# Performance work log

Hardware: AMD Instinct MI355X
Metric: run time of the kernel (lower is better)

The kernel has to match this reference:

```python
import jax, jax.numpy as jnp
import numpy as np

N_NODES = 10000
N_EDGES = 160000
HIDDEN = 128
NGAUSS = 100
NF = 64
N_CONV = 2


def setup_inputs() -> dict:
    key = jax.random.key(0)
    ks = jax.random.split(key, 10)
    h = jax.random.normal(ks[0], (N_NODES, HIDDEN), dtype=jnp.float32)
    edge_index = jax.random.randint(ks[1], (2, N_EDGES), 0, N_NODES, dtype=jnp.int64)
    edge_weight = jax.random.uniform(ks[2], (N_EDGES,), dtype=jnp.float32)
    edge_attr = jax.random.normal(ks[3], (N_EDGES, NGAUSS), dtype=jnp.float32)
    data = jnp.zeros((1,), dtype=jnp.float32)
    s = 0.05
    lin0_w = jax.random.normal(ks[4], (HIDDEN, NF), dtype=jnp.float32) * s
    lin0_b = jnp.zeros((NF,), dtype=jnp.float32)
    nn_w1 = jax.random.normal(ks[5], (NGAUSS, HIDDEN), dtype=jnp.float32) * s
    nn_b1 = jnp.zeros((HIDDEN,), dtype=jnp.float32)
    nn_w2 = jax.random.normal(ks[6], (HIDDEN, NF * NF), dtype=jnp.float32) * s
    nn_b2 = jnp.zeros((NF * NF,), dtype=jnp.float32)
    root_w = jax.random.normal(ks[7], (NF, NF), dtype=jnp.float32) * s
    conv_b = jnp.zeros((NF,), dtype=jnp.float32)
    return {"h": h, "edge_index": edge_index, "edge_weight": edge_weight,
            "edge_attr": edge_attr, "data": data,
            "lin0_w": lin0_w, "lin0_b": lin0_b,
            "nn_w1": nn_w1, "nn_b1": nn_b1, "nn_w2": nn_w2, "nn_b2": nn_b2,
            "root_w": root_w, "conv_b": conv_b}


def reference(h, edge_index, edge_weight, edge_attr, data,
              lin0_w, lin0_b, nn_w1, nn_b1, nn_w2, nn_b2, root_w, conv_b):
    # lin0 + relu -> node features x: [N, nf]
    x = jax.nn.relu(h @ lin0_w + lin0_b)

    # edge network: per-edge weight matrix W_e: [E, nf, nf]
    hidden = jax.nn.relu(edge_attr @ nn_w1 + nn_b1)
    W_e = (hidden @ nn_w2 + nn_b2).reshape(N_EDGES, NF, NF)

    src = edge_index[0]  # message source (x_j)
    dst = edge_index[1]  # aggregation target (i)

    # in-degree for mean aggregation (0-degree nodes -> 0 output)
    deg = jax.ops.segment_sum(jnp.ones((N_EDGES,), x.dtype), dst, num_segments=N_NODES)
    inv_deg = (1.0 / jnp.maximum(deg, 1.0))[:, None]  # [N, 1]

    # n_conv applications of the SAME NNConv (shared weights)
    for _ in range(N_CONV):
        msg = jnp.einsum('ei,eio->eo', x[src], W_e)  # gather + per-edge matvec
        agg = jax.ops.segment_sum(msg, dst, num_segments=N_NODES) * inv_deg
        x = agg + x @ root_w + conv_b
    return x
```

## Files before the change

### kernel.cpp

```cpp
#include <hip/hip_runtime.h>

#define N_NODES 10000
#define N_EDGES 160000
#define HID 128
#define NG 100
#define NF 64
#define NIO 4096
#define NJ 8192
#define M_PAD 10240

typedef short bf16x8 __attribute__((ext_vector_type(8)));
typedef float f32x4 __attribute__((ext_vector_type(4)));

__device__ __forceinline__ unsigned short f2b(float f) {
    unsigned int u = __float_as_uint(f);
    u += 0x7fffu + ((u >> 16) & 1u);
    return (unsigned short)(u >> 16);
}
__device__ __forceinline__ float b2f(unsigned short s) { return __uint_as_float((unsigned int)s << 16); }

__device__ __forceinline__ long fidx64(int row, int k) {
    return (long)(row >> 4) * 1024 + (k >> 5) * 512 + ((((k >> 3) & 3) * 16 + (row & 15))) * 8 + (k & 7);
}
__device__ __forceinline__ long fidx128(int row, int k) {
    return (long)(row >> 4) * 2048 + (k >> 5) * 512 + ((((k >> 3) & 3) * 16 + (row & 15))) * 8 + (k & 7);
}

__global__ void hist_kernel(const int* __restrict__ src, const int* __restrict__ dst,
                            float* __restrict__ deg, int* __restrict__ cnt) {
    int e = blockIdx.x * 256 + threadIdx.x;
    if (e < N_EDGES) {
        atomicAdd(&deg[dst[e]], 1.0f);
        atomicAdd(&cnt[src[e]], 1);
    }
}

#define SCAN_C 40
__global__ void scan_kernel(const int* __restrict__ cnt, const float* __restrict__ deg,
                            int* __restrict__ rowptr, float* __restrict__ invd) {
    __shared__ int wsum[4];
    int t = threadIdx.x, wv = t >> 6, l = t & 63;
    int base_i = t * SCAN_C;
    int loc[SCAN_C];
    int sum = 0;
#pragma unroll
    for (int j = 0; j < SCAN_C; ++j) {
        int g = base_i + j;
        int v = (g < N_NODES) ? cnt[g] : 0;
        loc[j] = sum;
        sum += v;
    }
    int incl = sum;
    for (int off = 1; off < 64; off <<= 1) {
        int v = __shfl_up(incl, off);
        if (l >= off) incl += v;
    }
    if (l == 63) wsum[wv] = incl;
    __syncthreads();
    int wbase = 0;
#pragma unroll
    for (int w = 0; w < 4; ++w) wbase += (w < wv) ? wsum[w] : 0;
    int tbase = wbase + incl - sum;
#pragma unroll
    for (int j = 0; j < SCAN_C; ++j) {
        int g = base_i + j;
        if (g <= N_NODES) rowptr[g] = tbase + loc[j];
        if (g < N_NODES) invd[g] = 1.0f / fmaxf(deg[g], 1.0f);
    }
}

__global__ void scatter_kernel(const int* __restrict__ src, const int* __restrict__ dst,
                               const int* __restrict__ rowptr, int* __restrict__ fill,
                               int* __restrict__ edgeOf, int* __restrict__ dstp) {
    int e = blockIdx.x * 256 + threadIdx.x;
    if (e < N_EDGES) {
        int s = src[e];
        int r = rowptr[s] + atomicAdd(&fill[s], 1);
        edgeOf[r] = e;
        dstp[r] = dst[e];
    }
}

__global__ void lin0_kernel(const float* __restrict__ h, const float* __restrict__ w,
                            const float* __restrict__ b, const float* __restrict__ b2,
                            float* __restrict__ x, unsigned short* __restrict__ xh,
                            float* __restrict__ xb2) {
    int wv = threadIdx.x >> 6, l = threadIdx.x & 63;
    int n = blockIdx.x * 4 + wv;
    float h0 = h[n * HID + l];
    float h1 = h[n * HID + 64 + l];
    float acc = b[l];
#pragma unroll
    for (int i = 0; i < 64; ++i) {
        acc += __shfl(h0, i) * w[i * NF + l];
        acc += __shfl(h1, i) * w[(64 + i) * NF + l];
    }
    float v = fmaxf(acc, 0.0f);
    x[n * NF + l] = v;
    xh[fidx64(n, l)] = f2b(v);
    float xb = 0.0f;
#pragma unroll
    for (int i = 0; i < 64; ++i) xb += __shfl(v, i) * b2[i * 64 + l];
    xb2[n * NF + l] = xb;
}

__global__ void eaperm_kernel(const float* __restrict__ ea, const int* __restrict__ edgeOf,
                              unsigned short* __restrict__ eah) {
    int t = threadIdx.x;
    int r15 = t & 15, ksl = t >> 4;
    int ks = ksl >> 2, lk = ksl & 3;
    long rank = (long)blockIdx.x * 16 + r15;
    long e = edgeOf[rank];
    int c0 = ks * 32 + lk * 8;
    unsigned int uh[4];
#pragma unroll
    for (int p = 0; p < 4; ++p) {
        float v0 = (c0 + 2 * p < NG) ? ea[e * NG + c0 + 2 * p] : 0.0f;
        float v1 = (c0 + 2 * p + 1 < NG) ? ea[e * NG + c0 + 2 * p + 1] : 0.0f;
        uh[p] = ((unsigned int)f2b(v1) << 16) | f2b(v0);
    }
    long idx = (long)blockIdx.x * 2048 + ks * 512 + (lk * 16 + r15) * 8;
    *(uint4*)(eah + idx) = make_uint4(uh[0], uh[1], uh[2], uh[3]);
}

__global__ void wpt_kernel(const float* __restrict__ w1, const float* __restrict__ w2,
                           unsigned short* __restrict__ w1h, unsigned short* __restrict__ w2h) {
    int id = blockIdx.x * 256 + threadIdx.x;
    if (id < HID * HID) {
        int k = id & 127, c = id >> 7;
        float v = (k < NG) ? w1[k * HID + c] : 0.0f;
        w1h[fidx128(c, k)] = f2b(v);
    } else {
        int id2 = id - HID * HID;
        int i = id2 & 63, j = id2 >> 6;
        int o = j >> 7, k = j & 127;
        w2h[fidx64(j, i)] = f2b(w2[k * NIO + i * 64 + o]);
    }
}

__launch_bounds__(256)
__global__ void hgemm_kernel(const unsigned short* __restrict__ eah,
                             const unsigned short* __restrict__ w1h,
                             const float* __restrict__ b1, unsigned short* __restrict__ hidp) {
    __shared__ float stg[4][1056];
    const int tid = threadIdx.x, wv = tid >> 6, l = tid & 63;
    const long grow = (long)blockIdx.x * 128;
    const int wr = (wv >> 1) * 64, wc = (wv & 1) * 64;
    const long apan0 = (grow >> 4) + (wr >> 4);
    const long bpan0 = (wc >> 4);

    f32x4 acc[4][4] = {};
#pragma unroll
    for (int ks = 0; ks < 4; ++ks) {
        bf16x8 a[4], b[4];
#pragma unroll
        for (int m = 0; m < 4; ++m)
            a[m] = *(const bf16x8*)(eah + (apan0 + m) * 2048 + ks * 512 + (long)l * 8);
#pragma unroll
        for (int n = 0; n < 4; ++n)
            b[n] = *(const bf16x8*)(w1h + (bpan0 + n) * 2048 + ks * 512 + (long)l * 8);
#pragma unroll
        for (int m = 0; m < 4; ++m)
#pragma unroll
            for (int n = 0; n < 4; ++n)
                acc[m][n] = __builtin_amdgcn_mfma_f32_16x16x32_bf16(a[m], b[n], acc[m][n], 0, 0, 0);
    }

    float* s = stg[wv];
    int r8 = l >> 3, cg = l & 7;
#pragma unroll
    for (int m = 0; m < 4; ++m) {
#pragma unroll
        for (int n = 0; n < 4; ++n)
#pragma unroll
            for (int q = 0; q < 4; ++q)
                s[((l >> 4) * 4 + q) * 66 + n * 16 + (l & 15)] = acc[m][n][q];
#pragma unroll
        for (int it = 0; it < 2; ++it) {
            int row = it * 8 + r8;
            const float* sr = s + row * 66 + cg * 8;
            int colbase = wc + cg * 8;
            unsigned int u[4];
#pragma unroll
            for (int p = 0; p < 4; ++p) {
                float f0 = fmaxf(sr[2 * p] + b1[colbase + 2 * p], 0.0f);
                float f1 = fmaxf(sr[2 * p + 1] + b1[colbase + 2 * p + 1], 0.0f);
                u[p] = ((unsigned int)f2b(f1) << 16) | f2b(f0);
            }
            long R = grow + wr + m * 16 + row;
            *(uint4*)(hidp + R * HID + colbase) = make_uint4(u[0], u[1], u[2], u[3]);
        }
    }
}

__launch_bounds__(256)
__global__ void ygemm_kernel(const unsigned short* __restrict__ xh,
                             const unsigned short* __restrict__ wh,
                             unsigned short* __restrict__ y, int n0) {
    __shared__ float stg[4][1056];
    const int tid = threadIdx.x, wv = tid >> 6, l = tid & 63;
    const int grow = blockIdx.x * 128;
    const int col0 = blockIdx.y * 128;
    const int wr = (wv >> 1) * 64, wc = (wv & 1) * 64;
    const long apan0 = ((n0 + grow + wr) >> 4);
    const long bpan0 = ((col0 + wc) >> 4);

    f32x4 acc[4][4] = {};
#pragma unroll
    for (int ks = 0; ks < 2; ++ks) {
        bf16x8 a[4], b[4];
#pragma unroll
        for (int m = 0; m < 4; ++m)
            a[m] = *(const bf16x8*)(xh + (apan0 + m) * 1024 + ks * 512 + (long)l * 8);
#pragma unroll
        for (int n = 0; n < 4; ++n)
            b[n] = *(const bf16x8*)(wh + (bpan0 + n) * 1024 + ks * 512 + (long)l * 8);
#pragma unroll
        for (int m = 0; m < 4; ++m)
#pragma unroll
            for (int n = 0; n < 4; ++n)
                acc[m][n] = __builtin_amdgcn_mfma_f32_16x16x32_bf16(a[m], b[n], acc[m][n], 0, 0, 0);
    }

    float* s = stg[wv];
    int r8 = l >> 3, cg = l & 7;
#pragma unroll
    for (int m = 0; m < 4; ++m) {
#pragma unroll
        for (int n = 0; n < 4; ++n)
#pragma unroll
            for (int q = 0; q < 4; ++q)
                s[((l >> 4) * 4 + q) * 66 + n * 16 + (l & 15)] = acc[m][n][q];
#pragma unroll
        for (int it = 0; it < 2; ++it) {
            int row = it * 8 + r8;
            const float* sr = s + row * 66 + cg * 8;
            unsigned int u[4];
#pragma unroll
            for (int p = 0; p < 4; ++p)
                u[p] = ((unsigned int)f2b(sr[2 * p + 1]) << 16) | f2b(sr[2 * p]);
            long R = grow + wr + m * 16 + row;
            *(uint4*)(y + R * NJ + col0 + wc + cg * 8) = make_uint4(u[0], u[1], u[2], u[3]);
        }
    }
}

__global__ void matvec_mfma_kernel(const unsigned short* __restrict__ y,
                                   const unsigned short* __restrict__ hidp,
                                   const int* __restrict__ rowptr, const int* __restrict__ dstp,
                                   const float* __restrict__ xb2, float* __restrict__ agg,
                                   int n0) {
    int wv = threadIdx.x >> 6, l = threadIdx.x & 63;
    int s = n0 + blockIdx.x;
    int r0 = rowptr[s], r1 = rowptr[s + 1];
    if (r0 == r1) return;
    int co = wv * 16;
    int lc = l & 15, lk = l >> 4;

    const unsigned short* Ys = y + (long)(s - n0) * NJ + (co + lc) * HID;
    bf16x8 b[4];
#pragma unroll
    for (int ks = 0; ks < 4; ++ks) b[ks] = *(const bf16x8*)(Ys + ks * 32 + lk * 8);
    float xb2v = xb2[(long)s * NF + co + lc];

    for (int mt = r0; mt < r1; mt += 16) {
        const unsigned short* Hs = hidp + (long)(mt + lc) * HID + lk * 8;
        f32x4 acc = {};
#pragma unroll
        for (int ks = 0; ks < 4; ++ks) {
            bf16x8 a = *(const bf16x8*)(Hs + ks * 32);
            acc = __builtin_amdgcn_mfma_f32_16x16x32_bf16(a, b[ks], acc, 0, 0, 0);
        }
#pragma unroll
        for (int q = 0; q < 4; ++q) {
            int rank = mt + lk * 4 + q;
            if (rank < r1) {
                int dd = dstp[rank];
                atomicAdd(&agg[(long)dd * NF + co + lc], acc[q] + xb2v);
            }
        }
    }
}

__global__ void combine_kernel(const float* __restrict__ x, const float* __restrict__ agg,
                               const float* __restrict__ invd, const float* __restrict__ rw,
                               const float* __restrict__ cb, const float* __restrict__ b2,
                               float* __restrict__ xo, unsigned short* __restrict__ xh,
                               float* __restrict__ xb2) {
    int wv = threadIdx.x >> 6, l = threadIdx.x & 63;
    int n = blockIdx.x * 4 + wv;
    float xv = x[n * NF + l];
    float acc = cb[l];
#pragma unroll
    for (int i = 0; i < 64; ++i) acc += __shfl(xv, i) * rw[i * NF + l];
    float v = agg[n * NF + l] * invd[n] + acc;
    xo[n * NF + l] = v;
    if (xh) {
        xh[fidx64(n, l)] = f2b(v);
        float xb = 0.0f;
#pragma unroll
        for (int i = 0; i < 64; ++i) xb += __shfl(v, i) * b2[i * 64 + l];
        xb2[n * NF + l] = xb;
    }
}

extern "C" void kernel_launch(void* const* d_in, const int* in_sizes, int n_in,
                              void* d_out, int out_size, void* d_ws, size_t ws_size,
                              hipStream_t stream) {
    const float* h = (const float*)d_in[0];
    const int* ei = (const int*)d_in[1];
    const float* ea = (const float*)d_in[3];
    const float* lin0_w = (const float*)d_in[5];
    const float* lin0_b = (const float*)d_in[6];
    const float* nn_w1 = (const float*)d_in[7];
    const float* nn_b1 = (const float*)d_in[8];
    const float* nn_w2 = (const float*)d_in[9];
    const float* nn_b2 = (const float*)d_in[10];
    const float* root_w = (const float*)d_in[11];
    const float* conv_b = (const float*)d_in[12];
    const int* srcIdx = ei;
    const int* dstIdx = ei + N_EDGES;

    const size_t eaBytes = (size_t)N_EDGES * HID * 2;
    const size_t fixed =
        (size_t)(N_EDGES + 16) * HID * 2 +
        (size_t)NJ * NF * 2 +
        (size_t)HID * HID * 2 +
        (size_t)M_PAD * NF * 2 +
        (size_t)N_NODES * NF * 4 * 4 +
        3 * 40192 +
        (size_t)N_NODES * 4 +
        (size_t)(N_NODES + 1) * 4 +
        (size_t)N_EDGES * 4 * 2 +
        32768;
    int nc = 0, CSn = 0;
    size_t region_bytes = 0;
    for (int c = 2; c <= 16; c *= 2) {
        int csn = (((N_NODES + c - 1) / c) + 127) & ~127;
        size_t rb = (size_t)csn * NJ * 2;
        if (rb < eaBytes) rb = eaBytes;
        if (fixed + rb <= ws_size) { nc = c; CSn = csn; region_bytes = rb; break; }
    }
    if (nc == 0) {
        hipMemsetAsync(d_out, 0, (size_t)out_size * 4, stream);
        return;
    }

    char* ws = (char*)d_ws;
    size_t off = 0;
    auto alloc = [&](size_t bytes) {
        char* p = ws + off;
        off += (bytes + 255) & ~(size_t)255;
        return p;
    };
    unsigned short* region = (unsigned short*)alloc(region_bytes);
    unsigned short* y = region;
    unsigned short* eah = region;
    unsigned short* hidp = (unsigned short*)alloc((size_t)(N_EDGES + 16) * HID * 2);
    unsigned short* w2h = (unsigned short*)alloc((size_t)NJ * NF * 2);
    unsigned short* w1h = (unsigned short*)alloc((size_t)HID * HID * 2);
    unsigned short* xh = (unsigned short*)alloc((size_t)M_PAD * NF * 2);
    float* xA = (float*)alloc((size_t)N_NODES * NF * 4);
    float* xB = (float*)alloc((size_t)N_NODES * NF * 4);
    float* agg = (float*)alloc((size_t)N_NODES * NF * 4);
    float* xb2 = (float*)alloc((size_t)N_NODES * NF * 4);
    char* degblk = alloc(3 * 40192);
    float* deg = (float*)degblk;
    int* cnt = (int*)(degblk + 40192);
    int* fill = (int*)(degblk + 2 * 40192);
    float* invd = (float*)alloc((size_t)N_NODES * 4);
    int* rowptr = (int*)alloc((size_t)(N_NODES + 1) * 4);
    int* edgeOf = (int*)alloc((size_t)N_EDGES * 4);
    int* dstp = (int*)alloc((size_t)N_EDGES * 4);

    hipMemsetAsync(degblk, 0, 3 * 40192, stream);
    hist_kernel<<<(N_EDGES + 255) / 256, 256, 0, stream>>>(srcIdx, dstIdx, deg, cnt);
    scan_kernel<<<1, 256, 0, stream>>>(cnt, deg, rowptr, invd);
    scatter_kernel<<<(N_EDGES + 255) / 256, 256, 0, stream>>>(srcIdx, dstIdx, rowptr, fill, edgeOf, dstp);
    lin0_kernel<<<N_NODES / 4, 256, 0, stream>>>(h, lin0_w, lin0_b, nn_b2, xA, xh, xb2);
    eaperm_kernel<<<N_EDGES / 16, 256, 0, stream>>>(ea, edgeOf, eah);
    wpt_kernel<<<(HID * HID + NJ * NF) / 256, 256, 0, stream>>>(nn_w1, nn_w2, w1h, w2h);
    hgemm_kernel<<<N_EDGES / 128, 256, 0, stream>>>(eah, w1h, nn_b1, hidp);

    for (int conv = 0; conv < 2; ++conv) {
        const float* xin = conv ? xB : xA;
        float* xout = conv ? (float*)d_out : xB;
        unsigned short* mh = conv ? nullptr : xh;

        hipMemsetAsync(agg, 0, (size_t)N_NODES * NF * 4, stream);
        for (int c = 0; c < nc; ++c) {
            int n0 = c * CSn;
            int n1 = n0 + CSn; if (n1 > N_NODES) n1 = N_NODES;
            if (n0 >= N_NODES) break;
            int gx = (n1 - n0 + 127) / 128;
            ygemm_kernel<<<dim3(gx, NJ / 128), 256, 0, stream>>>(xh, w2h, y, n0);
            matvec_mfma_kernel<<<n1 - n0, 256, 0, stream>>>(y, hidp, rowptr, dstp, xb2, agg, n0);
        }
        combine_kernel<<<N_NODES / 4, 256, 0, stream>>>(xin, agg, invd, root_w, conv_b, nn_b2,
                                                        xout, mh, xb2);
    }
}
```

Before: 371.5 us.

## Fuse per-node weight GEMM and edge matvec into one panel kernel

Replaces the chunked ygemm plus matvec launch pairs with a single kernel of 157 blocks. Each block computes the y (per-node projected weight) rows for a 64-node panel across all 8192 columns, then runs the MFMA matvec and atomic scatter for those same nodes. The aim is to remove per-chunk launch overhead and to reuse freshly written y data from cache. The cost is far less parallelism: fewer blocks than compute units, the column tiles and nodes are processed serially inside each block, and a full-size y buffer is required in the workspace.

```diff
diff --git a/kernel.cpp b/kernel.cpp
--- a/kernel.cpp
+++ b/kernel.cpp
@@ -8,6 +8,7 @@
 #define NIO 4096
 #define NJ 8192
 #define M_PAD 10240
+#define NPANEL 157
 
 typedef short bf16x8 __attribute__((ext_vector_type(8)));
 typedef float f32x4 __attribute__((ext_vector_type(4)));
@@ -194,89 +195,86 @@
 }
 
 __launch_bounds__(256)
-__global__ void ygemm_kernel(const unsigned short* __restrict__ xh,
-                             const unsigned short* __restrict__ wh,
-                             unsigned short* __restrict__ y, int n0) {
+__global__ void conv_fused_kernel(const unsigned short* __restrict__ xh,
+                                  const unsigned short* __restrict__ w2h,
+                                  const unsigned short* __restrict__ hidp,
+                                  const int* __restrict__ rowptr, const int* __restrict__ dstp,
+                                  const float* __restrict__ xb2, float* __restrict__ agg,
+                                  unsigned short* __restrict__ y) {
     __shared__ float stg[4][1056];
     const int tid = threadIdx.x, wv = tid >> 6, l = tid & 63;
-    const int grow = blockIdx.x * 128;
-    const int col0 = blockIdx.y * 128;
-    const int wr = (wv >> 1) * 64, wc = (wv & 1) * 64;
-    const long apan0 = ((n0 + grow + wr) >> 4);
-    const long bpan0 = ((col0 + wc) >> 4);
-
-    f32x4 acc[4][4] = {};
-#pragma unroll
-    for (int ks = 0; ks < 2; ++ks) {
-        bf16x8 a[4], b[4];
-#pragma unroll
-        for (int m = 0; m < 4; ++m)
-            a[m] = *(const bf16x8*)(xh + (apan0 + m) * 1024 + ks * 512 + (long)l * 8);
-#pragma unroll
-        for (int n = 0; n < 4; ++n)
-            b[n] = *(const bf16x8*)(wh + (bpan0 + n) * 1024 + ks * 512 + (long)l * 8);
-#pragma unroll
-        for (int m = 0; m < 4; ++m)
+    const int p0 = blockIdx.x * 64;
+    const long apan0 = (p0 >> 4);
+    const int r8 = l >> 3, cg = l & 7;
+
+    for (int ct = 0; ct < 32; ++ct) {
+        const int colW = ct * 256 + wv * 64;
+        const long bpan0 = (colW >> 4);
+        f32x4 acc[4][4] = {};
+#pragma unroll
+        for (int ks = 0; ks < 2; ++ks) {
+            bf16x8 a[4], b[4];
+#pragma unroll
+            for (int m = 0; m < 4; ++m)
+                a[m] = *(const bf16x8*)(xh + (apan0 + m) * 1024 + ks * 512 + (long)l * 8);
 #pragma unroll
             for (int n = 0; n < 4; ++n)
-                acc[m][n] = __builtin_amdgcn_mfma_f32_16x16x32_bf16(a[m], b[n], acc[m][n], 0, 0, 0);
-    }
-
-    float* s = stg[wv];
-    int r8 = l >> 3, cg = l & 7;
-#pragma unroll
-    for (int m = 0; m < 4; ++m) {
-#pragma unroll
-        for (int n = 0; n < 4; ++n)
-#pragma unroll
-            for (int q = 0; q < 4; ++q)
-                s[((l >> 4) * 4 + q) * 66 + n * 16 + (l & 15)] = acc[m][n][q];
-#pragma unroll
-        for (int it = 0; it < 2; ++it) {
-            int row = it * 8 + r8;
-            const float* sr = s + row * 66 + cg * 8;
-            unsigned int u[4];
-#pragma unroll
-            for (int p = 0; p < 4; ++p)
-                u[p] = ((unsigned int)f2b(sr[2 * p + 1]) << 16) | f2b(sr[2 * p]);
-            long R = grow + wr + m * 16 + row;
-            *(uint4*)(y + R * NJ + col0 + wc + cg * 8) = make_uint4(u[0], u[1], u[2], u[3]);
+                b[n] = *(const bf16x8*)(w2h + (bpan0 + n) * 1024 + ks * 512 + (long)l * 8);
+#pragma unroll
+            for (int m = 0; m < 4; ++m)
+#pragma unroll
+                for (int n = 0; n < 4; ++n)
+                    acc[m][n] = __builtin_amdgcn_mfma_f32_16x16x32_bf16(a[m], b[n], acc[m][n], 0, 0, 0);
         }
-    }
-}
-
-__global__ void matvec_mfma_kernel(const unsigned short* __restrict__ y,
-                                   const unsigned short* __restrict__ hidp,
-                                   const int* __restrict__ rowptr, const int* __restrict__ dstp,
-                                   const float* __restrict__ xb2, float* __restrict__ agg,
-                                   int n0) {
-    int wv = threadIdx.x >> 6, l = threadIdx.x & 63;
-    int s = n0 + blockIdx.x;
-    int r0 = rowptr[s], r1 = rowptr[s + 1];
-    if (r0 == r1) return;
-    int co = wv * 16;
-    int lc = l & 15, lk = l >> 4;
-
-    const unsigned short* Ys = y + (long)(s - n0) * NJ + (co + lc) * HID;
-    bf16x8 b[4];
-#pragma unroll
-    for (int ks = 0; ks < 4; ++ks) b[ks] = *(const bf16x8*)(Ys + ks * 32 + lk * 8);
-    float xb2v = xb2[(long)s * NF + co + lc];
-
-    for (int mt = r0; mt < r1; mt += 16) {
-        const unsigned short* Hs = hidp + (long)(mt + lc) * HID + lk * 8;
-        f32x4 acc = {};
-#pragma unroll
-        for (int ks = 0; ks < 4; ++ks) {
-            bf16x8 a = *(const bf16x8*)(Hs + ks * 32);
-            acc = __builtin_amdgcn_mfma_f32_16x16x32_bf16(a, b[ks], acc, 0, 0, 0);
+        float* s = stg[wv];
+#pragma unroll
+        for (int m = 0; m < 4; ++m) {
+#pragma unroll
+            for (int n = 0; n < 4; ++n)
+#pragma unroll
+                for (int q = 0; q < 4; ++q)
+                    s[((l >> 4) * 4 + q) * 66 + n * 16 + (l & 15)] = acc[m][n][q];
+#pragma unroll
+            for (int it = 0; it < 2; ++it) {
+                int row = it * 8 + r8;
+                const float* sr = s + row * 66 + cg * 8;
+                unsigned int u[4];
+#pragma unroll
+                for (int p = 0; p < 4; ++p)
+                    u[p] = ((unsigned int)f2b(sr[2 * p + 1]) << 16) | f2b(sr[2 * p]);
+                long R = p0 + m * 16 + row;
+                *(uint4*)(y + R * NJ + colW + cg * 8) = make_uint4(u[0], u[1], u[2], u[3]);
+            }
         }
-#pragma unroll
-        for (int q = 0; q < 4; ++q) {
-            int rank = mt + lk * 4 + q;
-            if (rank < r1) {
-                int dd = dstp[rank];
-                atomicAdd(&agg[(long)dd * NF + co + lc], acc[q] + xb2v);
+    }
+    __syncthreads();
+
+    const int co = wv * 16;
+    const int lc = l & 15, lk = l >> 4;
+    for (int sn = p0; sn < p0 + 64 && sn < N_NODES; ++sn) {
+        int r0 = rowptr[sn], r1 = rowptr[sn + 1];
+        if (r0 == r1) continue;
+        const unsigned short* Ys = y + (long)sn * NJ + (co + lc) * HID;
+        bf16x8 b[4];
+#pragma unroll
+        for (int ks = 0; ks < 4; ++ks) b[ks] = *(const bf16x8*)(Ys + ks * 32 + lk * 8);
+        float xb2v = xb2[(long)sn * NF + co + lc];
+
+        for (int mt = r0; mt < r1; mt += 16) {
+            const unsigned short* Hs = hidp + (long)(mt + lc) * HID + lk * 8;
+            f32x4 acc = {};
+#pragma unroll
+            for (int ks = 0; ks < 4; ++ks) {
+                bf16x8 a = *(const bf16x8*)(Hs + ks * 32);
+                acc = __builtin_amdgcn_mfma_f32_16x16x32_bf16(a, b[ks], acc, 0, 0, 0);
+            }
+#pragma unroll
+            for (int q = 0; q < 4; ++q) {
+                int rank = mt + lk * 4 + q;
+                if (rank < r1) {
+                    int dd = dstp[rank];
+                    atomicAdd(&agg[(long)dd * NF + co + lc], acc[q] + xb2v);
+                }
             }
         }
     }
@@ -322,6 +320,8 @@
     const int* dstIdx = ei + N_EDGES;
 
     const size_t eaBytes = (size_t)N_EDGES * HID * 2;
+    const size_t yBytes = (size_t)(NPANEL * 64) * NJ * 2;
+    size_t region_bytes = yBytes > eaBytes ? yBytes : eaBytes;
     const size_t fixed =
         (size_t)(N_EDGES + 16) * HID * 2 +
         (size_t)NJ * NF * 2 +
@@ -333,15 +333,7 @@
         (size_t)(N_NODES + 1) * 4 +
         (size_t)N_EDGES * 4 * 2 +
         32768;
-    int nc = 0, CSn = 0;
-    size_t region_bytes = 0;
-    for (int c = 2; c <= 16; c *= 2) {
-        int csn = (((N_NODES + c - 1) / c) + 127) & ~127;
-        size_t rb = (size_t)csn * NJ * 2;
-        if (rb < eaBytes) rb = eaBytes;
-        if (fixed + rb <= ws_size) { nc = c; CSn = csn; region_bytes = rb; break; }
-    }
-    if (nc == 0) {
+    if (fixed + region_bytes > ws_size) {
         hipMemsetAsync(d_out, 0, (size_t)out_size * 4, stream);
         return;
     }
@@ -388,14 +380,7 @@
         unsigned short* mh = conv ? nullptr : xh;
 
         hipMemsetAsync(agg, 0, (size_t)N_NODES * NF * 4, stream);
-        for (int c = 0; c < nc; ++c) {
-            int n0 = c * CSn;
-            int n1 = n0 + CSn; if (n1 > N_NODES) n1 = N_NODES;
-            if (n0 >= N_NODES) break;
-            int gx = (n1 - n0 + 127) / 128;
-            ygemm_kernel<<<dim3(gx, NJ / 128), 256, 0, stream>>>(xh, w2h, y, n0);
-            matvec_mfma_kernel<<<n1 - n0, 256, 0, stream>>>(y, hidp, rowptr, dstp, xb2, agg, n0);
-        }
+        conv_fused_kernel<<<NPANEL, 256, 0, stream>>>(xh, w2h, hidp, rowptr, dstp, xb2, agg, y);
         combine_kernel<<<N_NODES / 4, 256, 0, stream>>>(xin, agg, invd, root_w, conv_b, nn_b2,
                                                         xout, mh, xb2);
     }
```

New measurement: 722.4 us. 1.94x slower.
